# Optimization experiments

Hardware: AMD Instinct MI355X
Metric: run time of the kernel (lower is better)

The kernel has to match this reference:

```python
import jax, jax.numpy as jnp
import numpy as np

N = 50000
E = 800000
IN_DIM = 512
HID = 512
MLP_HID = 200
N_CLASSES = 2
BN_EPS = 1e-5


def setup_inputs() -> dict:
    key = jax.random.key(0)
    ks = jax.random.split(key, 12)
    def glorot(k, shape):
        fan_in, fan_out = shape[0], shape[1]
        lim = (6.0 / (fan_in + fan_out)) ** 0.5
        return jax.random.uniform(k, shape, jnp.float32, -lim, lim)
    return {
        "features": jax.random.normal(ks[0], (N, IN_DIM), jnp.float32),
        "src": jax.random.randint(ks[1], (E,), 0, N),
        "dst": jax.random.randint(ks[2], (E,), 0, N),
        # SAGEConv layer 1 & 2 (gcn aggregator -> only fc_neigh)
        "W1": glorot(ks[3], (IN_DIM, HID)),
        "b1": jnp.zeros((HID,), jnp.float32),
        "W2": glorot(ks[4], (HID, HID)),
        "b2": jnp.zeros((HID,), jnp.float32),
        # MLP predictor: Linear -> ReLU -> BatchNorm1d -> Linear
        "Wh": glorot(ks[5], (HID, MLP_HID)),
        "bh": jnp.zeros((MLP_HID,), jnp.float32),
        "gamma": jnp.ones((MLP_HID,), jnp.float32),
        "beta": jnp.zeros((MLP_HID,), jnp.float32),
        "Wo": glorot(ks[6], (MLP_HID, N_CLASSES)),
        "bo": jnp.zeros((N_CLASSES,), jnp.float32),
    }


def _sage_gcn_layer(h, src, dst, deg, W, b):
    # dgl.add_self_loop(g) + SAGEConv(aggregator_type='gcn'):
    # neigh_sum over (edges + self-loop) = segment_sum + h;
    # gcn aggregator then adds h_self once more and divides by (in_deg_with_selfloop + 1):
    #   h_neigh = (segment_sum(h[src]) + 2*h) / (deg_orig + 2)
    agg = jax.ops.segment_sum(h[src], dst, num_segments=h.shape[0])
    h_neigh = (agg + 2.0 * h) / (deg + 2.0)[:, None]
    # fc_neigh then activation=relu (fc commutes with the convex aggregation,
    # applied post-aggregation for clarity)
    return jax.nn.relu(h_neigh @ W + b)


def reference(features, src, dst, W1, b1, W2, b2, Wh, bh, gamma, beta, Wo, bo):
    n = features.shape[0]
    deg = jax.ops.segment_sum(jnp.ones_like(src, dtype=features.dtype), dst, num_segments=n)
    h = _sage_gcn_layer(features, src, dst, deg, W1, b1)  # dropout = identity (eval)
    h = _sage_gcn_layer(h, src, dst, deg, W2, b2)
    # MLP predictor (dropout identity): Linear -> ReLU -> BatchNorm1d -> Linear
    h = jax.nn.relu(h @ Wh + bh)
    mean = jnp.mean(h, axis=0)
    var = jnp.var(h, axis=0)  # biased var, matching torch BatchNorm training fwd
    h = (h - mean) * jax.lax.rsqrt(var + BN_EPS) * gamma + beta
    return h @ Wo + bo
```

## Files before the change

kernel.cpp:

```cpp
#include <hip/hip_runtime.h>

#define NN 50000
#define NE 800000
#define DIM 512
#define MLPH 200

typedef __attribute__((ext_vector_type(8))) short short8;
typedef __attribute__((ext_vector_type(4))) float f32x4;

#define GL2LDS(g, l)                                                     \
    __builtin_amdgcn_global_load_lds(                                    \
        (const __attribute__((address_space(1))) unsigned int*)(g),      \
        (__attribute__((address_space(3))) unsigned int*)(l), 16, 0, 0)

__device__ inline unsigned short f2bf(float f) {
    unsigned int u = __float_as_uint(f);
    unsigned int r = (u + 0x7fffu + ((u >> 16) & 1u)) >> 16;
    return (unsigned short)r;
}
__device__ inline float bflo(unsigned u) { return __uint_as_float(u << 16); }
__device__ inline float bfhi(unsigned u) { return __uint_as_float(u & 0xffff0000u); }
__device__ inline unsigned pack2(float a, float b) {
    return (unsigned)f2bf(a) | ((unsigned)f2bf(b) << 16);
}

__global__ void k_hist(const int* __restrict__ dst, int* __restrict__ counts) {
    int e = blockIdx.x * blockDim.x + threadIdx.x;
    if (e < NE) atomicAdd(&counts[dst[e]], 1);
}

__global__ void k_part(const int* __restrict__ counts, int* __restrict__ partial) {
    int t = threadIdx.x;
    int i = blockIdx.x * 256 + t;
    int x = (i < NN) ? counts[i] : 0;
#pragma unroll
    for (int off = 32; off; off >>= 1) x += __shfl_down(x, off);
    __shared__ int ws[4];
    if ((t & 63) == 0) ws[t >> 6] = x;
    __syncthreads();
    if (t == 0) partial[blockIdx.x] = ws[0] + ws[1] + ws[2] + ws[3];
}

__global__ void k_scanp(int* __restrict__ partial, int* __restrict__ rowstart, int nb) {
    __shared__ int ws[4];
    int t = threadIdx.x;
    int x = (t < nb) ? partial[t] : 0;
    int v = x;
#pragma unroll
    for (int off = 1; off < 64; off <<= 1) {
        int u = __shfl_up(v, off);
        if ((t & 63) >= off) v += u;
    }
    if ((t & 63) == 63) ws[t >> 6] = v;
    __syncthreads();
    int add = 0;
#pragma unroll
    for (int w = 0; w < 4; w++)
        if (w < (t >> 6)) add += ws[w];
    if (t < nb) partial[t] = v - x + add;
    if (t == 255) rowstart[NN] = v + add;
}

__global__ void k_scan2(const int* __restrict__ counts, const int* __restrict__ pexcl,
                        int* __restrict__ rowstart, int* __restrict__ cursor) {
    __shared__ int ws[4];
    int t = threadIdx.x;
    int i = blockIdx.x * 256 + t;
    int x = (i < NN) ? counts[i] : 0;
    int v = x;
#pragma unroll
    for (int off = 1; off < 64; off <<= 1) {
        int u = __shfl_up(v, off);
        if ((t & 63) >= off) v += u;
    }
    if ((t & 63) == 63) ws[t >> 6] = v;
    __syncthreads();
    int add = 0;
#pragma unroll
    for (int w = 0; w < 4; w++)
        if (w < (t >> 6)) add += ws[w];
    if (i < NN) {
        int r = pexcl[blockIdx.x] + v - x + add;
        rowstart[i] = r;
        cursor[i] = r;
    }
}

__global__ void k_fill(const int* __restrict__ src, const int* __restrict__ dst,
                       int* __restrict__ cursor, int* __restrict__ adj) {
    int e = blockIdx.x * blockDim.x + threadIdx.x;
    if (e < NE) {
        int p = atomicAdd(&cursor[dst[e]], 1);
        adj[p] = src[e];
    }
}

__global__ void k_cvt(const float* __restrict__ in, ushort* __restrict__ out, int n4) {
    int i = blockIdx.x * blockDim.x + threadIdx.x;
    if (i >= n4) return;
    float4 v = *(const float4*)(in + (size_t)i * 4);
    ushort2 a{f2bf(v.x), f2bf(v.y)}, b{f2bf(v.z), f2bf(v.w)};
    *(ushort2*)(out + (size_t)i * 4) = a;
    *(ushort2*)(out + (size_t)i * 4 + 2) = b;
}

__global__ void k_wt3(const float* __restrict__ W1, const float* __restrict__ W2,
                      const float* __restrict__ Wh, ushort* __restrict__ W1t,
                      ushort* __restrict__ W2t, ushort* __restrict__ Wht) {
    int i = blockIdx.x * 256 + threadIdx.x;
    const int S1 = 512 * 512, S2 = 2 * 512 * 512, S3 = 2 * 512 * 512 + MLPH * 512;
    if (i < S1) {
        int n = i >> 9, k = i & 511;
        W1t[i] = f2bf(W1[(size_t)k * 512 + n]);
    } else if (i < S2) {
        int j = i - S1, n = j >> 9, k = j & 511;
        W2t[j] = f2bf(W2[(size_t)k * 512 + n]);
    } else if (i < S3) {
        int j = i - S2, n = j >> 9, k = j & 511;
        Wht[j] = f2bf(Wh[(size_t)k * MLPH + n]);
    }
}

__device__ inline void addrow(float* acc, uint4 v) {
    acc[0] += bflo(v.x); acc[1] += bfhi(v.x);
    acc[2] += bflo(v.y); acc[3] += bfhi(v.y);
    acc[4] += bflo(v.z); acc[5] += bfhi(v.z);
    acc[6] += bflo(v.w); acc[7] += bfhi(v.w);
}

__global__ __launch_bounds__(256) void k_agg_bf(const ushort* __restrict__ h,
                                                const int* __restrict__ rowstart,
                                                const int* __restrict__ adj,
                                                ushort* __restrict__ out) {
    int node = blockIdx.x * 4 + (threadIdx.x >> 6);
    int lane = threadIdx.x & 63;
    if (node >= NN) return;
    int s = rowstart[node], e = rowstart[node + 1];
    const size_t coff = (size_t)lane * 8;
    float acc[8];
    {
        uint4 v = *(const uint4*)(h + (size_t)node * DIM + coff);
        acc[0] = 2.f * bflo(v.x); acc[1] = 2.f * bfhi(v.x);
        acc[2] = 2.f * bflo(v.y); acc[3] = 2.f * bfhi(v.y);
        acc[4] = 2.f * bflo(v.z); acc[5] = 2.f * bfhi(v.z);
        acc[6] = 2.f * bflo(v.w); acc[7] = 2.f * bfhi(v.w);
    }
    int i = s;
    int e4 = s + ((e - s) & ~3);
    for (; i < e4; i += 4) {
        int n0 = adj[i], n1 = adj[i + 1], n2 = adj[i + 2], n3 = adj[i + 3];
        uint4 v0 = *(const uint4*)(h + (size_t)n0 * DIM + coff);
        uint4 v1 = *(const uint4*)(h + (size_t)n1 * DIM + coff);
        uint4 v2 = *(const uint4*)(h + (size_t)n2 * DIM + coff);
        uint4 v3 = *(const uint4*)(h + (size_t)n3 * DIM + coff);
        addrow(acc, v0);
        addrow(acc, v1);
        addrow(acc, v2);
        addrow(acc, v3);
    }
    for (; i < e; i++) {
        int nbr = adj[i];
        uint4 v = *(const uint4*)(h + (size_t)nbr * DIM + coff);
        addrow(acc, v);
    }
    float inv = 1.0f / (float)(e - s + 2);
    uint4 o;
    o.x = pack2(acc[0] * inv, acc[1] * inv);
    o.y = pack2(acc[2] * inv, acc[3] * inv);
    o.z = pack2(acc[4] * inv, acc[5] * inv);
    o.w = pack2(acc[6] * inv, acc[7] * inv);
    *(uint4*)(out + (size_t)node * DIM + coff) = o;
}

template <int NCOLS, int OMODE>
__global__ __launch_bounds__(256) void k_ggemm(const ushort* __restrict__ A,
                                               const ushort* __restrict__ Bt,
                                               const float* __restrict__ bias,
                                               float* __restrict__ Cf,
                                               ushort* __restrict__ Cb, int M) {
    constexpr int K = 512;
    constexpr int NT = K / 32;
    __shared__ ushort As[2][128 * 32];
    __shared__ ushort Bs[2][128 * 32];
    const int tid = threadIdx.x;
    const int wid = tid >> 6, lane = tid & 63;
    const int wm = wid >> 1, wn = wid & 1;
    const int col0 = blockIdx.x * 128;
    const int row0 = blockIdx.y * 128;
    const int l15 = lane & 15, lk = (lane >> 4) * 8;

    const int sbase = wid * 32;
    const int lrow = lane >> 2;
    const int lseg = (lane & 3) * 8;

    auto stage = [&](int buf, int k0) {
#pragma unroll
        for (int j = 0; j < 2; j++) {
            const int r = sbase + j * 16;
            int gr = row0 + r + lrow;
            if (gr > M - 1) gr = M - 1;
            GL2LDS(A + (size_t)gr * K + k0 + lseg, &As[buf][r * 32]);
            int gc = col0 + r + lrow;
            if (NCOLS % 128 != 0) {
                if (gc > NCOLS - 1) gc = NCOLS - 1;
            }
            GL2LDS(Bt + (size_t)gc * K + k0 + lseg, &Bs[buf][r * 32]);
        }
    };

    f32x4 acc[4][4] = {};
    stage(0, 0);
    __syncthreads();
    for (int t = 0; t < NT; ++t) {
        const int cur = t & 1;
        if (t + 1 < NT) stage(cur ^ 1, (t + 1) * 32);
        short8 a[4], b[4];
#pragma unroll
        for (int m = 0; m < 4; m++)
            a[m] = *(const short8*)(&As[cur][(wm * 64 + m * 16 + l15) * 32 + lk]);
#pragma unroll
        for (int n = 0; n < 4; n++)
            b[n] = *(const short8*)(&Bs[cur][(wn * 64 + n * 16 + l15) * 32 + lk]);
#pragma unroll
        for (int m = 0; m < 4; m++)
#pragma unroll
            for (int n = 0; n < 4; n++)
                acc[m][n] = __builtin_amdgcn_mfma_f32_16x16x32_bf16(a[m], b[n], acc[m][n], 0, 0, 0);
        __syncthreads();
    }

    const int crow = row0 + wm * 64;
    const int ccol = col0 + wn * 64;
#pragma unroll
    for (int n = 0; n < 4; n++) {
        int c = ccol + n * 16 + l15;
        if (NCOLS % 128 != 0 && c >= NCOLS) continue;
        float bv = bias[c];
#pragma unroll
        for (int m = 0; m < 4; m++) {
#pragma unroll
            for (int i = 0; i < 4; i++) {
                int r = crow + m * 16 + (lane >> 4) * 4 + i;
                if (r >= M) continue;
                float v = fmaxf(acc[m][n][i] + bv, 0.0f);
                if (OMODE == 0) Cf[(size_t)r * NCOLS + c] = v;
                else Cb[(size_t)r * NCOLS + c] = f2bf(v);
            }
        }
    }
}

__global__ void k_bnstat(const float* __restrict__ hm, float* __restrict__ gsum,
                         float* __restrict__ gsq) {
    int j = threadIdx.x;
    if (j >= MLPH) return;
    float s = 0.f, q = 0.f;
    for (int r = blockIdx.x; r < NN; r += gridDim.x) {
        float v = hm[(size_t)r * MLPH + j];
        s += v;
        q += v * v;
    }
    atomicAdd(&gsum[j], s);
    atomicAdd(&gsq[j], q);
}

__global__ void k_bnfin(const float* __restrict__ gsum, const float* __restrict__ gsq,
                        const float* __restrict__ gamma, const float* __restrict__ beta,
                        const float* __restrict__ Wo, const float* __restrict__ bo,
                        float* __restrict__ Wo2, float* __restrict__ bo2) {
    __shared__ float sh[MLPH];
    int j = threadIdx.x;
    if (j < MLPH) {
        float mean = gsum[j] / (float)NN;
        float var = gsq[j] / (float)NN - mean * mean;
        float scale = gamma[j] * rsqrtf(var + 1e-5f);
        float shift = beta[j] - mean * scale;
        sh[j] = shift;
        Wo2[j * 2 + 0] = scale * Wo[j * 2 + 0];
        Wo2[j * 2 + 1] = scale * Wo[j * 2 + 1];
    }
    __syncthreads();
    if (j < 2) {
        float acc = bo[j];
        for (int t = 0; t < MLPH; t++) acc += sh[t] * Wo[t * 2 + j];
        bo2[j] = acc;
    }
}

__global__ void k_out(const float* __restrict__ hm, const float* __restrict__ Wo2,
                      const float* __restrict__ bo2, float* __restrict__ out) {
    __shared__ float w[MLPH * 2];
    if (threadIdx.x < MLPH * 2) w[threadIdx.x] = Wo2[threadIdx.x];
    __syncthreads();
    int wid = (blockIdx.x * blockDim.x + threadIdx.x) >> 6;
    int lane = threadIdx.x & 63;
    if (wid >= NN) return;
    const float* row = hm + (size_t)wid * MLPH;
    float p0 = 0.f, p1 = 0.f;
    for (int j = lane; j < MLPH; j += 64) {
        float v = row[j];
        p0 += v * w[j * 2 + 0];
        p1 += v * w[j * 2 + 1];
    }
    for (int off = 32; off; off >>= 1) {
        p0 += __shfl_down(p0, off);
        p1 += __shfl_down(p1, off);
    }
    if (lane == 0) {
        out[wid * 2 + 0] = p0 + bo2[0];
        out[wid * 2 + 1] = p1 + bo2[1];
    }
}

extern "C" void kernel_launch(void* const* d_in, const int* in_sizes, int n_in,
                              void* d_out, int out_size, void* d_ws, size_t ws_size,
                              hipStream_t stream) {
    const float* features = (const float*)d_in[0];
    const int* src = (const int*)d_in[1];
    const int* dst = (const int*)d_in[2];
    const float* W1 = (const float*)d_in[3];
    const float* b1 = (const float*)d_in[4];
    const float* W2 = (const float*)d_in[5];
    const float* b2 = (const float*)d_in[6];
    const float* Wh = (const float*)d_in[7];
    const float* bh = (const float*)d_in[8];
    const float* gamma = (const float*)d_in[9];
    const float* beta = (const float*)d_in[10];
    const float* Wo = (const float*)d_in[11];
    const float* bo = (const float*)d_in[12];
    float* out = (float*)d_out;

    char* w = (char*)d_ws;
    auto alloc = [&](size_t bytes) -> void* {
        void* p = (void*)w;
        w += (bytes + 255) & ~(size_t)255;
        return p;
    };
    ushort* fb = (ushort*)alloc((size_t)NN * DIM * 2);
    ushort* ab = (ushort*)alloc((size_t)NN * DIM * 2);
    ushort* hb = (ushort*)alloc((size_t)NN * DIM * 2);
    float* hm = (float*)alloc((size_t)NN * MLPH * 4);
    ushort* W1t = (ushort*)alloc((size_t)DIM * DIM * 2);
    ushort* W2t = (ushort*)alloc((size_t)DIM * DIM * 2);
    ushort* Wht = (ushort*)alloc((size_t)MLPH * DIM * 2);
    int* adj = (int*)alloc((size_t)NE * 4);
    int* counts = (int*)alloc((size_t)NN * 4);
    int* rowstart = (int*)alloc((size_t)(NN + 1) * 4);
    int* cursor = (int*)alloc((size_t)NN * 4);
    int* partial = (int*)alloc(256 * 4);
    float* gsum = (float*)alloc(MLPH * 4);
    float* gsq = (float*)alloc(MLPH * 4);
    float* Wo2 = (float*)alloc(MLPH * 2 * 4);
    float* bo2 = (float*)alloc(2 * 4);

    hipMemsetAsync(counts, 0, (size_t)NN * 4, stream);
    hipMemsetAsync(gsum, 0, MLPH * 4, stream);
    hipMemsetAsync(gsq, 0, MLPH * 4, stream);

    const int NB = (NN + 255) / 256;

    k_hist<<<(NE + 255) / 256, 256, 0, stream>>>(dst, counts);
    k_part<<<NB, 256, 0, stream>>>(counts, partial);
    k_scanp<<<1, 256, 0, stream>>>(partial, rowstart, NB);
    k_scan2<<<NB, 256, 0, stream>>>(counts, partial, rowstart, cursor);
    k_fill<<<(NE + 255) / 256, 256, 0, stream>>>(src, dst, cursor, adj);

    const int n4 = NN * DIM / 4;
    k_cvt<<<(n4 + 255) / 256, 256, 0, stream>>>(features, fb, n4);
    const int WT = 2 * 512 * 512 + MLPH * 512;
    k_wt3<<<(WT + 255) / 256, 256, 0, stream>>>(W1, W2, Wh, W1t, W2t, Wht);

    const int MB = (NN + 127) / 128;

    k_agg_bf<<<(NN + 3) / 4, 256, 0, stream>>>(fb, rowstart, adj, ab);
    k_ggemm<DIM, 1><<<dim3(4, MB), 256, 0, stream>>>(ab, W1t, b1, nullptr, hb, NN);
    k_agg_bf<<<(NN + 3) / 4, 256, 0, stream>>>(hb, rowstart, adj, ab);
    k_ggemm<DIM, 1><<<dim3(4, MB), 256, 0, stream>>>(ab, W2t, b2, nullptr, fb, NN);
    k_ggemm<MLPH, 0><<<dim3(2, MB), 256, 0, stream>>>(fb, Wht, bh, hm, nullptr, NN);
    k_bnstat<<<512, 256, 0, stream>>>(hm, gsum, gsq);
    k_bnfin<<<1, 256, 0, stream>>>(gsum, gsq, gamma, beta, Wo, bo, Wo2, bo2);
    k_out<<<(NN * 64 + 511) / 512, 512, 0, stream>>>(hm, Wo2, bo2, out);
}
```

Before: 604.4 us.

## Use 256-row GEMM tiles with XCD-aware block swizzle and nontemporal aggregation I/O

The GEMM kernel moves to 512-thread blocks that each compute a 256x128 tile, so every staged B tile is reused across twice as many rows. Launch is now a 1D grid whose block index is remapped so consecutive tiles land on the same XCD, which should improve L2 locality. The aggregation kernel uses nontemporal loads for the adjacency indices and a nontemporal store for its output, to keep those streams from evicting the gathered feature rows in cache. Risks are lower occupancy from the larger LDS footprint, and the swizzle assumes the grid size is a multiple of 8; the epilogue code is not visible, so it is unclear whether it was updated to match the new tile shape.

Measured after the change: 595.6 us. No clear change (-1.5%).

```diff
diff --git a/kernel.cpp b/kernel.cpp
--- a/kernel.cpp
+++ b/kernel.cpp
@@ -7,6 +7,7 @@
 
 typedef __attribute__((ext_vector_type(8))) short short8;
 typedef __attribute__((ext_vector_type(4))) float f32x4;
+typedef __attribute__((ext_vector_type(4))) unsigned int u32x4;
 
 #define GL2LDS(g, l)                                                     \
     __builtin_amdgcn_global_load_lds(                                    \
@@ -148,7 +149,10 @@
     int i = s;
     int e4 = s + ((e - s) & ~3);
     for (; i < e4; i += 4) {
-        int n0 = adj[i], n1 = adj[i + 1], n2 = adj[i + 2], n3 = adj[i + 3];
+        int n0 = __builtin_nontemporal_load(adj + i);
+        int n1 = __builtin_nontemporal_load(adj + i + 1);
+        int n2 = __builtin_nontemporal_load(adj + i + 2);
+        int n3 = __builtin_nontemporal_load(adj + i + 3);
         uint4 v0 = *(const uint4*)(h + (size_t)n0 * DIM + coff);
         uint4 v1 = *(const uint4*)(h + (size_t)n1 * DIM + coff);
         uint4 v2 = *(const uint4*)(h + (size_t)n2 * DIM + coff);
@@ -159,53 +163,57 @@
         addrow(acc, v3);
     }
     for (; i < e; i++) {
-        int nbr = adj[i];
+        int nbr = __builtin_nontemporal_load(adj + i);
         uint4 v = *(const uint4*)(h + (size_t)nbr * DIM + coff);
         addrow(acc, v);
     }
     float inv = 1.0f / (float)(e - s + 2);
-    uint4 o;
+    u32x4 o;
     o.x = pack2(acc[0] * inv, acc[1] * inv);
     o.y = pack2(acc[2] * inv, acc[3] * inv);
     o.z = pack2(acc[4] * inv, acc[5] * inv);
     o.w = pack2(acc[6] * inv, acc[7] * inv);
-    *(uint4*)(out + (size_t)node * DIM + coff) = o;
+    __builtin_nontemporal_store(o, (u32x4*)(out + (size_t)node * DIM + coff));
 }
 
 template <int NCOLS, int OMODE>
-__global__ __launch_bounds__(256) void k_ggemm(const ushort* __restrict__ A,
+__global__ __launch_bounds__(512) void k_ggemm(const ushort* __restrict__ A,
                                                const ushort* __restrict__ Bt,
                                                const float* __restrict__ bias,
                                                float* __restrict__ Cf,
                                                ushort* __restrict__ Cb, int M) {
     constexpr int K = 512;
     constexpr int NT = K / 32;
-    __shared__ ushort As[2][128 * 32];
+    constexpr int NC = (NCOLS + 127) / 128;
+    __shared__ ushort As[2][256 * 32];
     __shared__ ushort Bs[2][128 * 32];
     const int tid = threadIdx.x;
     const int wid = tid >> 6, lane = tid & 63;
     const int wm = wid >> 1, wn = wid & 1;
-    const int col0 = blockIdx.x * 128;
-    const int row0 = blockIdx.y * 128;
+
+    const int cpx = gridDim.x >> 3;
+    const int wg = (blockIdx.x & 7) * cpx + (blockIdx.x >> 3);
+    const int col0 = (wg % NC) * 128;
+    const int row0 = (wg / NC) * 256;
+
     const int l15 = lane & 15, lk = (lane >> 4) * 8;
-
-    const int sbase = wid * 32;
     const int lrow = lane >> 2;
     const int lseg = (lane & 3) * 8;
 
     auto stage = [&](int buf, int k0) {
 #pragma unroll
         for (int j = 0; j < 2; j++) {
-            const int r = sbase + j * 16;
+            const int r = wid * 16 + j * 128;
             int gr = row0 + r + lrow;
             if (gr > M - 1) gr = M - 1;
             GL2LDS(A + (size_t)gr * K + k0 + lseg, &As[buf][r * 32]);
-            int gc = col0 + r + lrow;
-            if (NCOLS % 128 != 0) {
-                if (gc > NCOLS - 1) gc = NCOLS - 1;
-            }
-            GL2LDS(Bt + (size_t)gc * K + k0 + lseg, &Bs[buf][r * 32]);
         }
+        const int rb = wid * 16;
+        int gc = col0 + rb + lrow;
+        if (NCOLS % 128 != 0) {
+            if (gc > NCOLS - 1) gc = NCOLS - 1;
+        }
+        GL2LDS(Bt + (size_t)gc * K + k0 + lseg, &Bs[buf][rb * 32]);
     };
 
     f32x4 acc[4][4] = {};
@@ -370,13 +378,15 @@
     const int WT = 2 * 512 * 512 + MLPH * 512;
     k_wt3<<<(WT + 255) / 256, 256, 0, stream>>>(W1, W2, Wh, W1t, W2t, Wht);
 
-    const int MB = (NN + 127) / 128;
+    const int MBr = (NN + 255) / 256;
+    const int G512 = 4 * MBr;
+    const int G200 = 2 * MBr;
 
     k_agg_bf<<<(NN + 3) / 4, 256, 0, stream>>>(fb, rowstart, adj, ab);
-    k_ggemm<DIM, 1><<<dim3(4, MB), 256, 0, stream>>>(ab, W1t, b1, nullptr, hb, NN);
+    k_ggemm<DIM, 1><<<G512, 512, 0, stream>>>(ab, W1t, b1, nullptr, hb, NN);
     k_agg_bf<<<(NN + 3) / 4, 256, 0, stream>>>(hb, rowstart, adj, ab);
-    k_ggemm<DIM, 1><<<dim3(4, MB), 256, 0, stream>>>(ab, W2t, b2, nullptr, fb, NN);
-    k_ggemm<MLPH, 0><<<dim3(2, MB), 256, 0, stream>>>(fb, Wht, bh, hm, nullptr, NN);
+    k_ggemm<DIM, 1><<<G512, 512, 0, stream>>>(ab, W2t, b2, nullptr, fb, NN);
+    k_ggemm<MLPH, 0><<<G200, 512, 0, stream>>>(fb, Wht, bh, hm, nullptr, NN);
     k_bnstat<<<512, 256, 0, stream>>>(hm, gsum, gsq);
     k_bnfin<<<1, 256, 0, stream>>>(gsum, gsq, gamma, beta, Wo, bo, Wo2, bo2);
     k_out<<<(NN * 64 + 511) / 512, 512, 0, stream>>>(hm, Wo2, bo2, out);
```
